# Performance work log

Hardware: AMD Instinct MI355X
Metric: run time of the kernel (lower is better)

The kernel has to match this reference:

```python
import jax, jax.numpy as jnp
import numpy as np


def fps_single(xyz, npoint):
    """Furthest point sampling. xyz: [N,3] -> [npoint] int32 indices (first = 0)."""
    d0 = jnp.sum((xyz - xyz[0]) ** 2, axis=-1)  # [N]

    def body(dists, _):
        nxt = jnp.argmax(dists)
        d = jnp.sum((xyz - xyz[nxt]) ** 2, axis=-1)
        return jnp.minimum(dists, d), nxt.astype(jnp.int32)

    _, idxs = jax.lax.scan(body, d0, None, length=npoint - 1)
    return jnp.concatenate([jnp.zeros((1,), jnp.int32), idxs])


def setup_inputs() -> dict:
    key = jax.random.key(0)
    k1, k2 = jax.random.split(key)
    B, N, C = 4, 8192, 128
    points = jax.random.normal(k1, (B, N, 3), dtype=jnp.float32)
    features = jax.random.normal(k2, (B, C, N), dtype=jnp.float32)
    return {"points": points, "features": features, "npoint": 2048, "nsample": 16}


def reference(points, features, npoint, nsample):
    """FPS downsample -> kNN grouping (mean pool) -> three_nn inverse-distance interpolation.
    points: [B,N,3], features: [B,C,N]. Returns interpolated features [B,C,N]."""
    B, N, _ = points.shape
    # --- furthest point sampling (Sample module) ---
    fps_idx = jax.vmap(lambda p: fps_single(p, npoint))(points)          # [B,Q]
    xyz_q = jnp.take_along_axis(points, fps_idx[..., None], axis=1)      # [B,Q,3]
    # --- pairwise squared distances query->all (pdist2squared) ---
    sq = (jnp.sum(xyz_q ** 2, -1)[:, :, None]
          + jnp.sum(points ** 2, -1)[:, None, :]
          - 2.0 * jnp.einsum('bqd,bnd->bqn', xyz_q, points))             # [B,Q,N]
    sq = jnp.maximum(sq, 0.0)
    # --- kNN neighbors, drop self (SampleNeighbors, knn=True takes topk nsample+1 then [:,:,1:]) ---
    _, nbr = jax.lax.top_k(-sq, nsample + 1)                             # [B,Q,K+1]
    nbr = nbr[..., 1:]                                                   # [B,Q,K]
    grouped = jax.vmap(lambda f, idx: f[:, idx])(features, nbr)          # [B,C,Q,K]
    coarse = jnp.mean(grouped, axis=-1)                                  # [B,C,Q]
    # --- three_nn + inverse squared-distance interpolation (GraphFPModule) ---
    neg_d3, i3 = jax.lax.top_k(-jnp.swapaxes(sq, 1, 2), 3)               # [B,N,3]
    d3 = jnp.maximum(-neg_d3, 1e-10)                                     # squared dists, clamped
    inv = 1.0 / (d3 + 1e-8)
    w = inv / jnp.sum(inv, axis=-1, keepdims=True)                       # [B,N,3]
    f3 = jax.vmap(lambda f, idx: f[:, idx])(coarse, i3)                  # [B,C,N,3]
    out = jnp.sum(f3 * w[:, None, :, :], axis=-1)                        # [B,C,N]
    return out
```

## Files before the change

### kernel.cpp

```cpp
#include <hip/hip_runtime.h>
#include <cstdint>
#include <cstddef>

#define Bq   4
#define Nq   8192
#define Cq   128
#define NPq  2048
#define KSEL 17

typedef float v2f __attribute__((ext_vector_type(2)));

__device__ __forceinline__ float rn_sq3(float x, float y, float z) {
  return __fadd_rn(__fadd_rn(__fmul_rn(x, x), __fmul_rn(y, y)), __fmul_rn(z, z));
}

__device__ __forceinline__ v2f dist2_v2(v2f px, v2f py, v2f pz, float cx, float cy, float cz) {
#pragma clang fp contract(off)
  v2f dx = px - cx;
  v2f dy = py - cy;
  v2f dz = pz - cz;
  v2f s = dx * dx + dy * dy + dz * dz;
  return s;
}

__device__ __forceinline__ float sq_expand(float qx, float qy, float qz, float sq_,
                                           float px, float py, float pz, float sp_) {
  float dot = __fadd_rn(__fadd_rn(__fmul_rn(qx, px), __fmul_rn(qy, py)), __fmul_rn(qz, pz));
  float v = __fsub_rn(__fadd_rn(sq_, sp_), __fmul_rn(2.0f, dot));
  v = fmaxf(v, 0.0f);
  return __fadd_rn(v, 0.0f);
}

__global__ __launch_bounds__(256) void k_sump(const float* __restrict__ pts,
                                              float* __restrict__ sump,
                                              float4* __restrict__ pxyzs) {
  int g = blockIdx.x * 256 + threadIdx.x;
  float x = pts[g * 3 + 0], y = pts[g * 3 + 1], z = pts[g * 3 + 2];
  float s = rn_sq3(x, y, z);
  sump[g] = s;
  pxyzs[g] = make_float4(x, y, z, s);
}

template <int CTRL, int RM, int BM>
__device__ __forceinline__ float dpp_maxf(float v) {
  int r = __builtin_amdgcn_update_dpp(__float_as_int(v), __float_as_int(v), CTRL, RM, BM, false);
  return fmaxf(v, __int_as_float(r));
}

__global__ __launch_bounds__(512) void k_fps(const float* __restrict__ pts,
                                             int* __restrict__ fps_idx) {
  const int b = blockIdx.x;
  const int tid = threadIdx.x;
  const int lane = tid & 63, wid = tid >> 6;
  const float* P = pts + (size_t)b * Nq * 3;

  __shared__ float ldsx[Nq], ldsy[Nq], ldsz[Nq];
  __shared__ float sv[2][8];
  __shared__ int spi[2][8];

  v2f px[8], py[8], pz[8], dd[8];
  const int pbase = tid * 16;
#pragma unroll
  for (int j = 0; j < 8; j++) {
    const float2* q2 = (const float2*)(P + (size_t)(pbase + 2 * j) * 3);
    float2 A = q2[0], Bv = q2[1], Cv = q2[2];
    v2f tx, ty, tz;
    tx.x = A.x;  tx.y = Bv.y;
    ty.x = A.y;  ty.y = Cv.x;
    tz.x = Bv.x; tz.y = Cv.y;
    px[j] = tx; py[j] = ty; pz[j] = tz;
    ldsx[pbase + 2 * j] = tx.x; ldsx[pbase + 2 * j + 1] = tx.y;
    ldsy[pbase + 2 * j] = ty.x; ldsy[pbase + 2 * j + 1] = ty.y;
    ldsz[pbase + 2 * j] = tz.x; ldsz[pbase + 2 * j + 1] = tz.y;
  }
  float qx = P[0], qy = P[1], qz = P[2];
  v2f bdv;
  bdv.x = -1.0f; bdv.y = -1.0f;
#pragma unroll
  for (int j = 0; j < 8; j++) {
    v2f s = dist2_v2(px[j], py[j], pz[j], qx, qy, qz);
    dd[j] = s;
    bdv.x = fmaxf(bdv.x, s.x);
    bdv.y = fmaxf(bdv.y, s.y);
  }
  float bd = fmaxf(bdv.x, bdv.y);
  if (tid == 0) fps_idx[b * NPq] = 0;

  for (int i = 1; i < NPq; i++) {
    float wv = bd;
    wv = dpp_maxf<0x111, 0xf, 0xf>(wv);
    wv = dpp_maxf<0x112, 0xf, 0xf>(wv);
    wv = dpp_maxf<0x114, 0xf, 0xf>(wv);
    wv = dpp_maxf<0x118, 0xf, 0xf>(wv);
    wv = dpp_maxf<0x142, 0xa, 0xf>(wv);
    wv = dpp_maxf<0x143, 0xc, 0xf>(wv);
    float wmax = __int_as_float(__builtin_amdgcn_readlane(__float_as_int(wv), 63));
    unsigned long long msk = __ballot(bd == wmax);
    int wl = (int)__ffsll(msk) - 1;
    if (lane == wl) {
      int kk = 15;
#pragma unroll
      for (int j = 7; j >= 0; j--) {
        if (dd[j].y == wmax) kk = 2 * j + 1;
        if (dd[j].x == wmax) kk = 2 * j;
      }
      sv[i & 1][wid] = wmax;
      spi[i & 1][wid] = pbase + kk;
    }
    __syncthreads();

    float v = sv[i & 1][lane & 7];
    int slot = lane & 7;
#pragma unroll
    for (int off = 1; off < 8; off <<= 1) {
      float ov = __shfl_xor(v, off);
      int os = __shfl_xor(slot, off);
      bool take = (ov > v) || (ov == v && os < slot);
      v = take ? ov : v;
      slot = take ? os : slot;
    }
    int bip = spi[i & 1][slot];
    if (tid == 0) fps_idx[b * NPq + i] = bip;

    float cx = ldsx[bip], cy = ldsy[bip], cz = ldsz[bip];

    bdv.x = -1.0f; bdv.y = -1.0f;
#pragma unroll
    for (int j = 0; j < 8; j++) {
      v2f s = dist2_v2(px[j], py[j], pz[j], cx, cy, cz);
      v2f nd;
      nd.x = fminf(dd[j].x, s.x);
      nd.y = fminf(dd[j].y, s.y);
      dd[j] = nd;
      bdv.x = fmaxf(bdv.x, nd.x);
      bdv.y = fmaxf(bdv.y, nd.y);
    }
    bd = fmaxf(bdv.x, bdv.y);
  }
}

__global__ __launch_bounds__(256) void k_gatherq(const float* __restrict__ pts,
                                                 const float* __restrict__ sump,
                                                 const int* __restrict__ fps_idx,
                                                 float* __restrict__ xyzq,
                                                 float* __restrict__ sumq,
                                                 float* __restrict__ xqs,
                                                 float* __restrict__ yqs,
                                                 float* __restrict__ zqs) {
  int g = blockIdx.x * 256 + threadIdx.x;
  int b = g >> 11;
  int idx = fps_idx[g];
  int src = b * Nq + idx;
  float x = pts[src * 3 + 0], y = pts[src * 3 + 1], z = pts[src * 3 + 2];
  xyzq[g * 3 + 0] = x;
  xyzq[g * 3 + 1] = y;
  xyzq[g * 3 + 2] = z;
  xqs[g] = x; yqs[g] = y; zqs[g] = z;
  sumq[g] = sump[src];
}

__global__ __launch_bounds__(256) void k_knn_group(const float4* __restrict__ pxyzs,
                                                   const float* __restrict__ xyzq,
                                                   const float* __restrict__ sumq,
                                                   const float* __restrict__ feats,
                                                   float* __restrict__ coarse_t) {
  const int blk = blockIdx.x;
  const int b = blk >> 11;
  const int tid = threadIdx.x;
  const int lane = tid & 63, wid = tid >> 6;
  const float4* PS = pxyzs + (size_t)b * Nq;

  __shared__ float sq_lds[Nq];
  __shared__ unsigned long long wk[2][4];
  __shared__ int sel[KSEL];

  float qx = xyzq[blk * 3 + 0], qy = xyzq[blk * 3 + 1], qz = xyzq[blk * 3 + 2];
  float sq_ = sumq[blk];

  unsigned long long lmin = ~0ull;
#pragma unroll
  for (int k = 0; k < 32; k++) {
    int p = k * 256 + tid;
    float4 t = PS[p];
    float v = sq_expand(qx, qy, qz, sq_, t.x, t.y, t.z, t.w);
    sq_lds[p] = v;
    unsigned long long key = ((unsigned long long)__float_as_uint(v) << 32) | (unsigned int)p;
    lmin = key < lmin ? key : lmin;
  }

  for (int r = 0; r < KSEL; r++) {
    unsigned long long key = lmin;
#pragma unroll
    for (int off = 32; off > 0; off >>= 1) {
      unsigned long long o = __shfl_down(key, off);
      key = o < key ? o : key;
    }
    if (lane == 0) wk[r & 1][wid] = key;
    __syncthreads();
    unsigned long long m = wk[r & 1][0];
    m = wk[r & 1][1] < m ? wk[r & 1][1] : m;
    m = wk[r & 1][2] < m ? wk[r & 1][2] : m;
    m = wk[r & 1][3] < m ? wk[r & 1][3] : m;
    int p = (int)(unsigned int)(m & 0xFFFFFFFFull);
    if (tid == 0) sel[r] = p;
    if ((p & 255) == tid) {
      sq_lds[p] = __uint_as_float(0x7f800000u);
      lmin = ~0ull;
#pragma unroll
      for (int k = 0; k < 32; k++) {
        int pp = k * 256 + tid;
        unsigned long long kk =
            ((unsigned long long)__float_as_uint(sq_lds[pp]) << 32) | (unsigned int)pp;
        lmin = kk < lmin ? kk : lmin;
      }
    }
  }
  __syncthreads();

  if (tid < Cq) {
    const float* F = feats + ((size_t)(b * Cq + tid)) * Nq;
    float acc = 0.0f;
#pragma unroll
    for (int j = 1; j < KSEL; j++) acc += F[sel[j]];
    coarse_t[(size_t)blk * Cq + tid] = acc * (1.0f / 16.0f);
  }
}

__device__ __forceinline__ void merge3(unsigned long long& a0, unsigned long long& a1,
                                       unsigned long long& a2, unsigned long long b0,
                                       unsigned long long b1, unsigned long long b2) {
  unsigned long long lo1 = a0 < b0 ? a0 : b0;
  unsigned long long hi1 = a0 < b0 ? b0 : a0;
  unsigned long long lo2 = a1 < b1 ? a1 : b1;
  unsigned long long hi2 = a1 < b1 ? b1 : a1;
  unsigned long long lo3 = a2 < b2 ? a2 : b2;
  unsigned long long c1 = hi1 < lo2 ? hi1 : lo2;
  unsigned long long m1 = hi1 < lo2 ? lo2 : hi1;
  unsigned long long m2 = hi2 < lo3 ? hi2 : lo3;
  a0 = lo1;
  a1 = c1;
  a2 = m1 < m2 ? m1 : m2;
}

__global__ __launch_bounds__(256) void k_three(const float* __restrict__ pts,
                                               const float* __restrict__ sump,
                                               const float* __restrict__ xqs,
                                               const float* __restrict__ yqs,
                                               const float* __restrict__ zqs,
                                               const float* __restrict__ sumq,
                                               int* __restrict__ i0, int* __restrict__ i1,
                                               int* __restrict__ i2, float* __restrict__ w0,
                                               float* __restrict__ w1, float* __restrict__ w2) {
  const int wid = threadIdx.x >> 6, lane = threadIdx.x & 63;
  const int n = blockIdx.x * 4 + wid;
  const int b = n >> 13;
  float px = pts[n * 3 + 0], py = pts[n * 3 + 1], pz = pts[n * 3 + 2];
  float sp = sump[n];
  const float* QX = xqs + (size_t)b * NPq;
  const float* QY = yqs + (size_t)b * NPq;
  const float* QZ = zqs + (size_t)b * NPq;
  const float* SQ = sumq + (size_t)b * NPq;

  unsigned long long k0 = ~0ull, k1 = ~0ull, k2 = ~0ull;
#pragma unroll 4
  for (int j = 0; j < 32; j++) {
    int q = lane + j * 64;
    float v = sq_expand(QX[q], QY[q], QZ[q], SQ[q], px, py, pz, sp);
    unsigned long long key = ((unsigned long long)__float_as_uint(v) << 32) | (unsigned int)q;
    if (key < k2) {
      if (key < k1) {
        k2 = k1;
        if (key < k0) { k1 = k0; k0 = key; } else { k1 = key; }
      } else {
        k2 = key;
      }
    }
  }
#pragma unroll
  for (int off = 32; off > 0; off >>= 1) {
    unsigned long long o0 = __shfl_down(k0, off);
    unsigned long long o1 = __shfl_down(k1, off);
    unsigned long long o2 = __shfl_down(k2, off);
    merge3(k0, k1, k2, o0, o1, o2);
  }
  if (lane == 0) {
    float v0 = __uint_as_float((unsigned int)(k0 >> 32));
    float v1 = __uint_as_float((unsigned int)(k1 >> 32));
    float v2 = __uint_as_float((unsigned int)(k2 >> 32));
    float d0 = fmaxf(v0, 1e-10f), d1 = fmaxf(v1, 1e-10f), d2 = fmaxf(v2, 1e-10f);
    float inv0 = 1.0f / (d0 + 1e-8f);
    float inv1 = 1.0f / (d1 + 1e-8f);
    float inv2 = 1.0f / (d2 + 1e-8f);
    float s = inv0 + inv1 + inv2;
    i0[n] = (int)(unsigned int)(k0 & 0xFFFFFFFFull);
    i1[n] = (int)(unsigned int)(k1 & 0xFFFFFFFFull);
    i2[n] = (int)(unsigned int)(k2 & 0xFFFFFFFFull);
    w0[n] = inv0 / s;
    w1[n] = inv1 / s;
    w2[n] = inv2 / s;
  }
}

__global__ __launch_bounds__(256) void k_interp(const float* __restrict__ coarse_t,
                                                const int* __restrict__ i0,
                                                const int* __restrict__ i1,
                                                const int* __restrict__ i2,
                                                const float* __restrict__ w0,
                                                const float* __restrict__ w1,
                                                const float* __restrict__ w2,
                                                float* __restrict__ out) {
  int g = blockIdx.x * 256 + threadIdx.x;
  int b = g >> 13, n = g & (Nq - 1);
  int a0 = i0[g], a1 = i1[g], a2 = i2[g];
  float u0 = w0[g], u1 = w1[g], u2 = w2[g];
  const float4* r0 = (const float4*)(coarse_t + ((size_t)b * NPq + a0) * Cq);
  const float4* r1 = (const float4*)(coarse_t + ((size_t)b * NPq + a1) * Cq);
  const float4* r2 = (const float4*)(coarse_t + ((size_t)b * NPq + a2) * Cq);
  float* O = out + (size_t)b * Cq * Nq + n;
#pragma unroll 4
  for (int cq = 0; cq < Cq / 4; cq++) {
    float4 f0 = r0[cq], f1 = r1[cq], f2 = r2[cq];
    float o0 = u0 * f0.x + u1 * f1.x + u2 * f2.x;
    float o1 = u0 * f0.y + u1 * f1.y + u2 * f2.y;
    float o2 = u0 * f0.z + u1 * f1.z + u2 * f2.z;
    float o3 = u0 * f0.w + u1 * f1.w + u2 * f2.w;
    O[(size_t)(cq * 4 + 0) * Nq] = o0;
    O[(size_t)(cq * 4 + 1) * Nq] = o1;
    O[(size_t)(cq * 4 + 2) * Nq] = o2;
    O[(size_t)(cq * 4 + 3) * Nq] = o3;
  }
}

extern "C" void kernel_launch(void* const* d_in, const int* in_sizes, int n_in,
                              void* d_out, int out_size, void* d_ws, size_t ws_size,
                              hipStream_t stream) {
  const float* pts = (const float*)d_in[0];
  const float* feats = (const float*)d_in[1];
  float* out = (float*)d_out;

  char* ws = (char*)d_ws;
  size_t off = 0;
  auto alloc = [&](size_t bytes) {
    void* p = ws + off;
    off += (bytes + 255) & ~(size_t)255;
    return p;
  };
  float* sump = (float*)alloc((size_t)Bq * Nq * 4);
  float4* pxyzs = (float4*)alloc((size_t)Bq * Nq * 16);
  int* fps_idx = (int*)alloc((size_t)Bq * NPq * 4);
  float* xyzq = (float*)alloc((size_t)Bq * NPq * 3 * 4);
  float* sumq = (float*)alloc((size_t)Bq * NPq * 4);
  float* coarse_t = (float*)alloc((size_t)Bq * NPq * Cq * 4);
  int* i0 = (int*)alloc((size_t)Bq * Nq * 4);
  int* i1 = (int*)alloc((size_t)Bq * Nq * 4);
  int* i2 = (int*)alloc((size_t)Bq * Nq * 4);
  float* w0 = (float*)alloc((size_t)Bq * Nq * 4);
  float* w1 = (float*)alloc((size_t)Bq * Nq * 4);
  float* w2 = (float*)alloc((size_t)Bq * Nq * 4);
  float* xqs = (float*)alloc((size_t)Bq * NPq * 4);
  float* yqs = (float*)alloc((size_t)Bq * NPq * 4);
  float* zqs = (float*)alloc((size_t)Bq * NPq * 4);

  k_sump<<<(Bq * Nq) / 256, 256, 0, stream>>>(pts, sump, pxyzs);
  k_fps<<<Bq, 512, 0, stream>>>(pts, fps_idx);
  k_gatherq<<<(Bq * NPq) / 256, 256, 0, stream>>>(pts, sump, fps_idx, xyzq, sumq, xqs, yqs, zqs);
  k_knn_group<<<Bq * NPq, 256, 0, stream>>>(pxyzs, xyzq, sumq, feats, coarse_t);
  k_three<<<(Bq * Nq) / 4, 256, 0, stream>>>(pts, sump, xqs, yqs, zqs, sumq, i0, i1, i2, w0, w1, w2);
  k_interp<<<(Bq * Nq) / 256, 256, 0, stream>>>(coarse_t, i0, i1, i2, w0, w1, w2, out);
}
```

Before: 2.520 ms.

## Shrink FPS block to 4 waves and broadcast winner coordinates via LDS slot

The furthest-point-sampling kernel now runs 256 threads with 32 points per thread, reading the precomputed float4 point array. The winning lane writes its max distance plus coordinates into a small shared slot, so the LDS coordinate arrays and the index-dependent LDS lookup go away. The cross-wave reduction becomes a 4-way compare instead of an 8-way shuffle tree. This aims to cut the per-iteration serial latency of the 2047-step loop, in exchange for doubling per-thread distance work and raising register pressure.

```diff
diff --git a/kernel.cpp b/kernel.cpp
--- a/kernel.cpp
+++ b/kernel.cpp
@@ -47,38 +47,31 @@
   return fmaxf(v, __int_as_float(r));
 }
 
-__global__ __launch_bounds__(512) void k_fps(const float* __restrict__ pts,
+__global__ __launch_bounds__(256) void k_fps(const float4* __restrict__ pxyzs,
                                              int* __restrict__ fps_idx) {
   const int b = blockIdx.x;
   const int tid = threadIdx.x;
   const int lane = tid & 63, wid = tid >> 6;
-  const float* P = pts + (size_t)b * Nq * 3;
-
-  __shared__ float ldsx[Nq], ldsy[Nq], ldsz[Nq];
-  __shared__ float sv[2][8];
-  __shared__ int spi[2][8];
-
-  v2f px[8], py[8], pz[8], dd[8];
-  const int pbase = tid * 16;
-#pragma unroll
-  for (int j = 0; j < 8; j++) {
-    const float2* q2 = (const float2*)(P + (size_t)(pbase + 2 * j) * 3);
-    float2 A = q2[0], Bv = q2[1], Cv = q2[2];
-    v2f tx, ty, tz;
-    tx.x = A.x;  tx.y = Bv.y;
-    ty.x = A.y;  ty.y = Cv.x;
-    tz.x = Bv.x; tz.y = Cv.y;
-    px[j] = tx; py[j] = ty; pz[j] = tz;
-    ldsx[pbase + 2 * j] = tx.x; ldsx[pbase + 2 * j + 1] = tx.y;
-    ldsy[pbase + 2 * j] = ty.x; ldsy[pbase + 2 * j + 1] = ty.y;
-    ldsz[pbase + 2 * j] = tz.x; ldsz[pbase + 2 * j + 1] = tz.y;
-  }
-  float qx = P[0], qy = P[1], qz = P[2];
+  const float4* PS = pxyzs + (size_t)b * Nq;
+
+  __shared__ float4 slot[2][4];
+
+  v2f px[16], py[16], pz[16], dd[16];
+  const int pbase = tid * 32;
+
+  float4 q0 = PS[0];
   v2f bdv;
   bdv.x = -1.0f; bdv.y = -1.0f;
 #pragma unroll
-  for (int j = 0; j < 8; j++) {
-    v2f s = dist2_v2(px[j], py[j], pz[j], qx, qy, qz);
+  for (int j = 0; j < 16; j++) {
+    float4 a = PS[pbase + 2 * j];
+    float4 c = PS[pbase + 2 * j + 1];
+    v2f tx, ty, tz;
+    tx.x = a.x; tx.y = c.x;
+    ty.x = a.y; ty.y = c.y;
+    tz.x = a.z; tz.y = c.z;
+    px[j] = tx; py[j] = ty; pz[j] = tz;
+    v2f s = dist2_v2(tx, ty, tz, q0.x, q0.y, q0.z);
     dd[j] = s;
     bdv.x = fmaxf(bdv.x, s.x);
     bdv.y = fmaxf(bdv.y, s.y);
@@ -97,36 +90,37 @@
     float wmax = __int_as_float(__builtin_amdgcn_readlane(__float_as_int(wv), 63));
     unsigned long long msk = __ballot(bd == wmax);
     int wl = (int)__ffsll(msk) - 1;
-    if (lane == wl) {
-      int kk = 15;
-#pragma unroll
-      for (int j = 7; j >= 0; j--) {
+    bool iamw = (lane == wl);
+    int bip = 0;
+    if (iamw) {
+      int kk = 31;
+#pragma unroll
+      for (int j = 15; j >= 0; j--) {
         if (dd[j].y == wmax) kk = 2 * j + 1;
         if (dd[j].x == wmax) kk = 2 * j;
       }
-      sv[i & 1][wid] = wmax;
-      spi[i & 1][wid] = pbase + kk;
+      bip = pbase + kk;
+      int jj = kk >> 1;
+      bool odd = (kk & 1) != 0;
+      float cx = odd ? px[jj].y : px[jj].x;
+      float cy = odd ? py[jj].y : py[jj].x;
+      float cz = odd ? pz[jj].y : pz[jj].x;
+      slot[i & 1][wid] = make_float4(wmax, cx, cy, cz);
     }
     __syncthreads();
 
-    float v = sv[i & 1][lane & 7];
-    int slot = lane & 7;
-#pragma unroll
-    for (int off = 1; off < 8; off <<= 1) {
-      float ov = __shfl_xor(v, off);
-      int os = __shfl_xor(slot, off);
-      bool take = (ov > v) || (ov == v && os < slot);
-      v = take ? ov : v;
-      slot = take ? os : slot;
-    }
-    int bip = spi[i & 1][slot];
-    if (tid == 0) fps_idx[b * NPq + i] = bip;
-
-    float cx = ldsx[bip], cy = ldsy[bip], cz = ldsz[bip];
+    float4 s0 = slot[i & 1][0], s1 = slot[i & 1][1];
+    float4 s2 = slot[i & 1][2], s3 = slot[i & 1][3];
+    float bv = s0.x, cx = s0.y, cy = s0.z, cz = s0.w;
+    int ws = 0;
+    if (s1.x > bv) { bv = s1.x; cx = s1.y; cy = s1.z; cz = s1.w; ws = 1; }
+    if (s2.x > bv) { bv = s2.x; cx = s2.y; cy = s2.z; cz = s2.w; ws = 2; }
+    if (s3.x > bv) { bv = s3.x; cx = s3.y; cy = s3.z; cz = s3.w; ws = 3; }
+    if (iamw && wid == ws) fps_idx[b * NPq + i] = bip;
 
     bdv.x = -1.0f; bdv.y = -1.0f;
 #pragma unroll
-    for (int j = 0; j < 8; j++) {
+    for (int j = 0; j < 16; j++) {
       v2f s = dist2_v2(px[j], py[j], pz[j], cx, cy, cz);
       v2f nd;
       nd.x = fminf(dd[j].x, s.x);
@@ -362,7 +356,7 @@
   float* zqs = (float*)alloc((size_t)Bq * NPq * 4);
 
   k_sump<<<(Bq * Nq) / 256, 256, 0, stream>>>(pts, sump, pxyzs);
-  k_fps<<<Bq, 512, 0, stream>>>(pts, fps_idx);
+  k_fps<<<Bq, 256, 0, stream>>>(pxyzs, fps_idx);
   k_gatherq<<<(Bq * NPq) / 256, 256, 0, stream>>>(pts, sump, fps_idx, xyzq, sumq, xqs, yqs, zqs);
   k_knn_group<<<Bq * NPq, 256, 0, stream>>>(pxyzs, xyzq, sumq, feats, coarse_t);
   k_three<<<(Bq * Nq) / 4, 256, 0, stream>>>(pts, sump, xqs, yqs, zqs, sumq, i0, i1, i2, w0, w1, w2);
```

Result: slower. 4.784 ms (+89.9%).
